# Optimization experiments

Measured on AMD Instinct MI355X. Metric: run time of the kernel, lower is better.

## Reference

```python
import jax, jax.numpy as jnp
import numpy as np

PAD_ID = 2


def _positional_encoding(seq_len, d_model, dtype):
    # pe[pos, i] = cos((pos+1)/10000**(i/d))      if i even
    #            = sin((pos+1)/10000**((i+1)/d))  if i odd
    i = jnp.arange(d_model)
    even = (i % 2) == 0
    exponent = jnp.where(even, i, i + 1).astype(jnp.float32) / d_model
    inv_div = 10000.0 ** (-exponent)                      # [d]
    pos = (jnp.arange(seq_len) + 1).astype(jnp.float32)   # [S]
    angle = pos[:, None] * inv_div[None, :]               # [S, d]
    pe = jnp.where(even[None, :], jnp.cos(angle), jnp.sin(angle))
    return pe.astype(dtype)


def setup_inputs() -> dict:
    key = jax.random.key(0)
    k1, k2, k3 = jax.random.split(key, 3)
    d_model, vocab = 1024, 32000
    x = jax.random.randint(k1, (8, 2048), 0, vocab, dtype=jnp.int32)
    weight = jax.random.normal(k2, (d_model, vocab), dtype=jnp.float32) * 0.02
    bias = jax.random.normal(k3, (d_model,), dtype=jnp.float32) * 0.02
    return {"x": x, "weight": weight, "bias": bias}


def reference(x, weight, bias):
    # one_hot(x) @ weight.T + bias  ==  gather columns of weight
    emb = jnp.take(weight.T, x, axis=0) + bias            # [B, S, d]
    B, S, d = emb.shape
    pe = _positional_encoding(S, d, emb.dtype)            # [S, d]
    emb = emb + pe[None, :, :]
    # input_mask[b, i, j] = (x[b, j] == PAD_ID), broadcast over rows i
    pad = (x == PAD_ID)                                   # [B, S]
    input_mask = jnp.broadcast_to(pad[:, None, :], (B, S, S))
    return emb, input_mask
```

## Files before the change

### kernel.cpp

```cpp
#include <hip/hip_runtime.h>
#include <math.h>

#define D_MODEL 1024
#define SEQ     2048
#define BATCH   8
#define VOCAB   32000
#define PAD_ID  2
#define NTOK    (BATCH * SEQ)
#define CAP     64

typedef float f32x4 __attribute__((ext_vector_type(4)));

#define INV_EXP_C (13.287712379549449f / 1024.0f)

__global__ __launch_bounds__(256) void pe_zero_kernel(float* __restrict__ pe,
                                                      int*   __restrict__ cnt) {
    const int s  = blockIdx.x;
    const int d0 = threadIdx.x * 4;
    const float pos = (float)(s + 1);

    const float inv0 = exp2f(-(float)(d0)     * INV_EXP_C);
    const float inv1 = exp2f(-(float)(d0 + 2) * INV_EXP_C);
    const float inv2 = exp2f(-(float)(d0 + 4) * INV_EXP_C);

    float s1, c1;
    sincosf(pos * inv1, &s1, &c1);

    f32x4 v;
    v.x = cosf(pos * inv0);
    v.y = s1;
    v.z = c1;
    v.w = sinf(pos * inv2);

    *(f32x4*)(pe + (size_t)s * D_MODEL + d0) = v;

    const int gid = blockIdx.x * 256 + threadIdx.x;
    if (gid < VOCAB) cnt[gid] = 0;
}

__global__ __launch_bounds__(256) void bucket_kernel(const int* __restrict__ x,
                                                     int* __restrict__ cnt,
                                                     int* __restrict__ idx) {
    const int i = blockIdx.x * 256 + threadIdx.x;
    const int tok = x[i];
    const int p = atomicAdd(&cnt[tok], 1);
    if (p < CAP) idx[tok * CAP + p] = i;
}

__global__ __launch_bounds__(256) void fused_emb_kernel(
        const float* __restrict__ w,
        const float* __restrict__ bias,
        const float* __restrict__ pe,
        const int*   __restrict__ cnt,
        const int*   __restrict__ idx,
        float*       __restrict__ emb) {
    __shared__ float tile[64][65];
    const int v0 = blockIdx.x * 64;
    const int d0 = blockIdx.y * 64;
    const int t  = threadIdx.x;

    {
        const int vx = (t & 15) * 4;
        const int dy = t >> 4;
        #pragma unroll
        for (int i = 0; i < 64; i += 16) {
            const int d = d0 + dy + i;
            const f32x4 val = *(const f32x4*)(w + (size_t)d * VOCAB + v0 + vx);
            const float bv = bias[d];
            tile[vx + 0][dy + i] = val.x + bv;
            tile[vx + 1][dy + i] = val.y + bv;
            tile[vx + 2][dy + i] = val.z + bv;
            tile[vx + 3][dy + i] = val.w + bv;
        }
    }
    __syncthreads();

    const int vl    = t >> 2;
    const int lane4 = t & 3;
    const int v     = v0 + vl;
    const int n     = min(cnt[v], CAP);

    for (int k = 0; k < n; ++k) {
        const int i = idx[v * CAP + k];
        const int s = i & (SEQ - 1);
        float* ebase = emb + (size_t)i * D_MODEL + d0;
        const float* pbase = pe + (size_t)s * D_MODEL + d0;
        #pragma unroll
        for (int j = 0; j < 4; ++j) {
            const int dl = lane4 * 4 + j * 16;
            f32x4 wv;
            wv.x = tile[vl][dl + 0];
            wv.y = tile[vl][dl + 1];
            wv.z = tile[vl][dl + 2];
            wv.w = tile[vl][dl + 3];
            const f32x4 pv = *(const f32x4*)(pbase + dl);
            f32x4 o;
            o.x = wv.x + pv.x;
            o.y = wv.y + pv.y;
            o.z = wv.z + pv.z;
            o.w = wv.w + pv.w;
            __builtin_nontemporal_store(o, (f32x4*)(ebase + dl));
        }
    }
}

__global__ __launch_bounds__(256) void mask_kernel(const int* __restrict__ x,
                                                   float* __restrict__ mask) {
    const int i0 = blockIdx.x * 8;
    const int b  = blockIdx.y;
    const int j0 = threadIdx.x * 8;

    const int4 xi0 = *(const int4*)(x + b * SEQ + j0);
    const int4 xi1 = *(const int4*)(x + b * SEQ + j0 + 4);

    f32x4 m0, m1;
    m0.x = (xi0.x == PAD_ID) ? 1.0f : 0.0f;
    m0.y = (xi0.y == PAD_ID) ? 1.0f : 0.0f;
    m0.z = (xi0.z == PAD_ID) ? 1.0f : 0.0f;
    m0.w = (xi0.w == PAD_ID) ? 1.0f : 0.0f;
    m1.x = (xi1.x == PAD_ID) ? 1.0f : 0.0f;
    m1.y = (xi1.y == PAD_ID) ? 1.0f : 0.0f;
    m1.z = (xi1.z == PAD_ID) ? 1.0f : 0.0f;
    m1.w = (xi1.w == PAD_ID) ? 1.0f : 0.0f;

    float* mbase = mask + ((size_t)b * SEQ + i0) * SEQ + j0;
    #pragma unroll
    for (int r = 0; r < 8; ++r) {
        __builtin_nontemporal_store(m0, (f32x4*)(mbase + (size_t)r * SEQ));
        __builtin_nontemporal_store(m1, (f32x4*)(mbase + (size_t)r * SEQ + 4));
    }
}

__global__ __launch_bounds__(256) void fallback_kernel(
        const int* __restrict__ x, const float* __restrict__ w,
        const float* __restrict__ bias, float* __restrict__ emb,
        float* __restrict__ mask) {
    const int s = blockIdx.x, b = blockIdx.y, t = threadIdx.x;
    const int tok = x[b * SEQ + s];
    const int d0 = t * 4;

    const float* wc = w + tok;
    const f32x4 bv = *(const f32x4*)(bias + d0);
    const float pos  = (float)(s + 1);
    const float inv0 = exp2f(-(float)(d0)     * INV_EXP_C);
    const float inv1 = exp2f(-(float)(d0 + 2) * INV_EXP_C);
    const float inv2 = exp2f(-(float)(d0 + 4) * INV_EXP_C);
    float s1, c1;
    sincosf(pos * inv1, &s1, &c1);

    f32x4 o;
    o.x = wc[(size_t)(d0 + 0) * VOCAB] + bv.x + cosf(pos * inv0);
    o.y = wc[(size_t)(d0 + 1) * VOCAB] + bv.y + s1;
    o.z = wc[(size_t)(d0 + 2) * VOCAB] + bv.z + c1;
    o.w = wc[(size_t)(d0 + 3) * VOCAB] + bv.w + sinf(pos * inv2);
    __builtin_nontemporal_store(o, (f32x4*)(emb + ((size_t)(b * SEQ + s)) * D_MODEL + d0));

    const int j0 = t * 8;
    const int4 xi0 = *(const int4*)(x + b * SEQ + j0);
    const int4 xi1 = *(const int4*)(x + b * SEQ + j0 + 4);
    f32x4 m0, m1;
    m0.x = (xi0.x == PAD_ID) ? 1.0f : 0.0f;
    m0.y = (xi0.y == PAD_ID) ? 1.0f : 0.0f;
    m0.z = (xi0.z == PAD_ID) ? 1.0f : 0.0f;
    m0.w = (xi0.w == PAD_ID) ? 1.0f : 0.0f;
    m1.x = (xi1.x == PAD_ID) ? 1.0f : 0.0f;
    m1.y = (xi1.y == PAD_ID) ? 1.0f : 0.0f;
    m1.z = (xi1.z == PAD_ID) ? 1.0f : 0.0f;
    m1.w = (xi1.w == PAD_ID) ? 1.0f : 0.0f;
    float* mrow = mask + ((size_t)b * SEQ + s) * SEQ + j0;
    __builtin_nontemporal_store(m0, (f32x4*)mrow);
    __builtin_nontemporal_store(m1, (f32x4*)(mrow + 4));
}

extern "C" void kernel_launch(void* const* d_in, const int* in_sizes, int n_in,
                              void* d_out, int out_size, void* d_ws, size_t ws_size,
                              hipStream_t stream) {
    const int*   x    = (const int*)d_in[0];
    const float* w    = (const float*)d_in[1];
    const float* bias = (const float*)d_in[2];

    float* emb  = (float*)d_out;
    float* mask = (float*)d_out + (size_t)BATCH * SEQ * D_MODEL;

    const size_t pe_f   = (size_t)SEQ * D_MODEL;
    const size_t cnt_o  = pe_f;
    const size_t idx_o  = cnt_o + VOCAB;
    const size_t need   = (idx_o + (size_t)VOCAB * CAP) * 4;

    dim3 block(256);

    if (ws_size >= need) {
        float* pe  = (float*)d_ws;
        int*   cnt = (int*)d_ws + cnt_o;
        int*   idx = (int*)d_ws + idx_o;

        pe_zero_kernel<<<dim3(SEQ), block, 0, stream>>>(pe, cnt);
        bucket_kernel<<<dim3(NTOK / 256), block, 0, stream>>>(x, cnt, idx);
        fused_emb_kernel<<<dim3(VOCAB / 64, D_MODEL / 64), block, 0, stream>>>(
            w, bias, pe, cnt, idx, emb);
        mask_kernel<<<dim3(SEQ / 8, BATCH), block, 0, stream>>>(x, mask);
    } else {
        fallback_kernel<<<dim3(SEQ, BATCH), block, 0, stream>>>(x, w, bias, emb, mask);
    }
}
```

Before: 350.8 us.

## Transpose weight to bf16 table with bias, then gather rows per token

Replaces the bucketing scheme (atomic counts plus per-vocab index lists) with a two-step approach. The full weight is transposed into a bf16 [vocab, d] table with the bias folded in, and a per-token kernel then gathers contiguous rows and adds the positional encoding. This removes the atomics and the divergent per-vocab loops, and it halves the bytes gathered. In exchange it adds a 64MB bf16 write and read. Storing the embedding values in bf16 also reduces output precision relative to the fp32 reference.

After: 354.4 us. No clear change (+1.0%).

```diff
diff --git a/kernel.cpp b/kernel.cpp
--- a/kernel.cpp
+++ b/kernel.cpp
@@ -6,15 +6,21 @@
 #define BATCH   8
 #define VOCAB   32000
 #define PAD_ID  2
-#define NTOK    (BATCH * SEQ)
-#define CAP     64
 
 typedef float f32x4 __attribute__((ext_vector_type(4)));
+typedef unsigned short u16;
 
 #define INV_EXP_C (13.287712379549449f / 1024.0f)
 
-__global__ __launch_bounds__(256) void pe_zero_kernel(float* __restrict__ pe,
-                                                      int*   __restrict__ cnt) {
+static __device__ inline u16 f2bf(float f) {
+    unsigned u = __float_as_uint(f);
+    return (u16)((u + 0x7FFFu + ((u >> 16) & 1u)) >> 16);
+}
+static __device__ inline float bf2f(u16 v) {
+    return __uint_as_float(((unsigned)v) << 16);
+}
+
+__global__ __launch_bounds__(256) void pe_kernel(float* __restrict__ pe) {
     const int s  = blockIdx.x;
     const int d0 = threadIdx.x * 4;
     const float pos = (float)(s + 1);
@@ -33,27 +39,12 @@
     v.w = sinf(pos * inv2);
 
     *(f32x4*)(pe + (size_t)s * D_MODEL + d0) = v;
-
-    const int gid = blockIdx.x * 256 + threadIdx.x;
-    if (gid < VOCAB) cnt[gid] = 0;
-}
-
-__global__ __launch_bounds__(256) void bucket_kernel(const int* __restrict__ x,
-                                                     int* __restrict__ cnt,
-                                                     int* __restrict__ idx) {
-    const int i = blockIdx.x * 256 + threadIdx.x;
-    const int tok = x[i];
-    const int p = atomicAdd(&cnt[tok], 1);
-    if (p < CAP) idx[tok * CAP + p] = i;
-}
-
-__global__ __launch_bounds__(256) void fused_emb_kernel(
+}
+
+__global__ __launch_bounds__(256) void transpose_bias_bf16_kernel(
         const float* __restrict__ w,
         const float* __restrict__ bias,
-        const float* __restrict__ pe,
-        const int*   __restrict__ cnt,
-        const int*   __restrict__ idx,
-        float*       __restrict__ emb) {
+        u16*         __restrict__ wT) {
     __shared__ float tile[64][65];
     const int v0 = blockIdx.x * 64;
     const int d0 = blockIdx.y * 64;
@@ -67,41 +58,50 @@
             const int d = d0 + dy + i;
             const f32x4 val = *(const f32x4*)(w + (size_t)d * VOCAB + v0 + vx);
             const float bv = bias[d];
-            tile[vx + 0][dy + i] = val.x + bv;
-            tile[vx + 1][dy + i] = val.y + bv;
-            tile[vx + 2][dy + i] = val.z + bv;
-            tile[vx + 3][dy + i] = val.w + bv;
+            tile[dy + i][vx + 0] = val.x + bv;
+            tile[dy + i][vx + 1] = val.y + bv;
+            tile[dy + i][vx + 2] = val.z + bv;
+            tile[dy + i][vx + 3] = val.w + bv;
         }
     }
     __syncthreads();
-
-    const int vl    = t >> 2;
-    const int lane4 = t & 3;
-    const int v     = v0 + vl;
-    const int n     = min(cnt[v], CAP);
-
-    for (int k = 0; k < n; ++k) {
-        const int i = idx[v * CAP + k];
-        const int s = i & (SEQ - 1);
-        float* ebase = emb + (size_t)i * D_MODEL + d0;
-        const float* pbase = pe + (size_t)s * D_MODEL + d0;
+    {
+        const int dx = (t & 15) * 4;
+        const int vy = t >> 4;
         #pragma unroll
-        for (int j = 0; j < 4; ++j) {
-            const int dl = lane4 * 4 + j * 16;
-            f32x4 wv;
-            wv.x = tile[vl][dl + 0];
-            wv.y = tile[vl][dl + 1];
-            wv.z = tile[vl][dl + 2];
-            wv.w = tile[vl][dl + 3];
-            const f32x4 pv = *(const f32x4*)(pbase + dl);
-            f32x4 o;
-            o.x = wv.x + pv.x;
-            o.y = wv.y + pv.y;
-            o.z = wv.z + pv.z;
-            o.w = wv.w + pv.w;
-            __builtin_nontemporal_store(o, (f32x4*)(ebase + dl));
+        for (int i = 0; i < 64; i += 16) {
+            ushort4 o;
+            o.x = f2bf(tile[dx + 0][vy + i]);
+            o.y = f2bf(tile[dx + 1][vy + i]);
+            o.z = f2bf(tile[dx + 2][vy + i]);
+            o.w = f2bf(tile[dx + 3][vy + i]);
+            *(ushort4*)(wT + (size_t)(v0 + vy + i) * D_MODEL + d0 + dx) = o;
         }
     }
+}
+
+__global__ __launch_bounds__(256) void emb_gather_kernel(
+        const int*   __restrict__ x,
+        const u16*   __restrict__ wT,
+        const float* __restrict__ pe,
+        float*       __restrict__ emb) {
+    const int s = blockIdx.x;
+    const int b = blockIdx.y;
+    const int d0 = threadIdx.x * 4;
+
+    const int tok = x[b * SEQ + s];
+
+    const ushort4 wv = *(const ushort4*)(wT + (size_t)tok * D_MODEL + d0);
+    const f32x4   pv = *(const f32x4*)(pe + (size_t)s * D_MODEL + d0);
+
+    f32x4 o;
+    o.x = bf2f(wv.x) + pv.x;
+    o.y = bf2f(wv.y) + pv.y;
+    o.z = bf2f(wv.z) + pv.z;
+    o.w = bf2f(wv.w) + pv.w;
+
+    __builtin_nontemporal_store(o,
+        (f32x4*)(emb + ((size_t)(b * SEQ + s)) * D_MODEL + d0));
 }
 
 __global__ __launch_bounds__(256) void mask_kernel(const int* __restrict__ x,
@@ -182,22 +182,20 @@
     float* emb  = (float*)d_out;
     float* mask = (float*)d_out + (size_t)BATCH * SEQ * D_MODEL;
 
-    const size_t pe_f   = (size_t)SEQ * D_MODEL;
-    const size_t cnt_o  = pe_f;
-    const size_t idx_o  = cnt_o + VOCAB;
-    const size_t need   = (idx_o + (size_t)VOCAB * CAP) * 4;
+    const size_t pe_f  = (size_t)SEQ * D_MODEL;
+    const size_t wt_e  = (size_t)VOCAB * D_MODEL;
+    const size_t need  = pe_f * 4 + wt_e * 2;
 
     dim3 block(256);
 
     if (ws_size >= need) {
-        float* pe  = (float*)d_ws;
-        int*   cnt = (int*)d_ws + cnt_o;
-        int*   idx = (int*)d_ws + idx_o;
-
-        pe_zero_kernel<<<dim3(SEQ), block, 0, stream>>>(pe, cnt);
-        bucket_kernel<<<dim3(NTOK / 256), block, 0, stream>>>(x, cnt, idx);
-        fused_emb_kernel<<<dim3(VOCAB / 64, D_MODEL / 64), block, 0, stream>>>(
-            w, bias, pe, cnt, idx, emb);
+        float* pe = (float*)d_ws;
+        u16*   wT = (u16*)((char*)d_ws + pe_f * 4);
+
+        pe_kernel<<<dim3(SEQ), block, 0, stream>>>(pe);
+        transpose_bias_bf16_kernel<<<dim3(VOCAB / 64, D_MODEL / 64), block, 0, stream>>>(
+            w, bias, wT);
+        emb_gather_kernel<<<dim3(SEQ, BATCH), block, 0, stream>>>(x, wT, pe, emb);
         mask_kernel<<<dim3(SEQ / 8, BATCH), block, 0, stream>>>(x, mask);
     } else {
         fallback_kernel<<<dim3(SEQ, BATCH), block, 0, stream>>>(x, w, bias, emb, mask);
```
